# Performance work log

Measured on AMD Instinct MI355X. Metric: run time of the kernel, lower is better.

Reference implementation:

```python
import jax, jax.numpy as jnp
import numpy as np
import math

D_MODEL = 1024
N_HEAD = 16
HEAD_DIM = D_MODEL // N_HEAD
SEQ_LEN = 512
INIT_SIZE = 1568  # from RelativeSinusoidalPositionalEmbedding default


def _rel_pos_embedding(seq_len, embedding_dim):
    # Replicates RelativeSinusoidalPositionalEmbedding with init_size=1568
    num_embeddings = INIT_SIZE + 1  # 1569
    half_dim = embedding_dim // 2
    scale = math.log(10000.0) / (half_dim - 1)
    freqs = np.exp(np.arange(half_dim, dtype=np.float32) * -scale)
    pos = np.arange(-(num_embeddings // 2), num_embeddings // 2, dtype=np.float32)  # [-785, 784)
    emb = pos[:, None] * freqs[None, :]
    weights = np.concatenate([np.sin(emb), np.cos(emb)], axis=1).astype(np.float32)  # (1569, d)
    weights[0, :] = 0.0  # padding_idx
    origin_shift = num_embeddings // 2 + 1  # 785
    positions = np.arange(-seq_len, seq_len) + origin_shift
    embed = weights[positions]  # (2*seq_len, d)
    return jnp.asarray(embed.T)  # (d, 2*seq_len), matching .T in __init__


def setup_inputs() -> dict:
    key = jax.random.key(0)
    k1, k2, k3, k4, k5 = jax.random.split(key, 5)
    x = jax.random.normal(k1, (8, SEQ_LEN, D_MODEL), dtype=jnp.float32)
    prev = jax.random.normal(k2, (8, N_HEAD, SEQ_LEN, SEQ_LEN), dtype=jnp.float32)
    # Linear(d_model, 3*d_model, bias=False): store as (d_model, 3*d_model) for x @ W
    Wqkv = jax.random.normal(k3, (D_MODEL, 3 * D_MODEL), dtype=jnp.float32) / math.sqrt(D_MODEL)
    r_r_bias = jax.random.normal(k4, (1, N_HEAD, 1, HEAD_DIM), dtype=jnp.float32) * 0.02
    r_w_bias = jax.random.normal(k5, (1, N_HEAD, 1, HEAD_DIM), dtype=jnp.float32) * 0.02
    rel_pos = _rel_pos_embedding(SEQ_LEN, HEAD_DIM)  # (head_dim, 2*seq_len)
    return {"x": x, "prev": prev, "Wqkv": Wqkv, "r_r_bias": r_r_bias,
            "r_w_bias": r_w_bias, "rel_pos": rel_pos, "skip_op": 1}


def _shift(BD, seq_len):
    # BD: (b, h, L, 2L) -> (b, h, L, L) via Transformer-XL pad/reshape trick
    b, h, L, two_L = BD.shape
    BD = jnp.pad(BD, ((0, 0), (0, 0), (0, 0), (0, 1)))        # (b,h,L,2L+1)
    BD = BD.reshape(b, h, -1, L)                               # (b,h,2L+1,L)
    BD = BD[:, :, :-1].reshape(b, h, L, -1)                    # (b,h,L,2L)
    return BD[:, :, :, seq_len:]                               # (b,h,L,L)


def reference(x, prev, Wqkv, r_r_bias, r_w_bias, rel_pos, skip_op):
    b, L, d = x.shape
    qkv = x @ Wqkv                                             # (b,L,3d)
    q, k, v = jnp.split(qkv, 3, axis=-1)
    q = q.reshape(b, L, N_HEAD, HEAD_DIM).transpose(0, 2, 1, 3)  # (b,h,L,hd)
    k = k.reshape(b, L, N_HEAD, HEAD_DIM).transpose(0, 2, 1, 3)
    v = v.reshape(b, L, N_HEAD, HEAD_DIM).transpose(0, 2, 1, 3)

    AC = jnp.einsum('bhqd,bhkd->bhqk', q + r_r_bias, k)
    BD = jnp.einsum('bhqd,dp->bhqp', q + r_w_bias, rel_pos)    # (b,h,L,2L)
    BD = _shift(BD, SEQ_LEN)
    E = jnp.einsum('bhkd,dp->bhkp', k, rel_pos)
    E = _shift(E, SEQ_LEN).transpose(0, 1, 3, 2)
    attn_score = (AC + BD + E) / math.sqrt(HEAD_DIM)
    if skip_op:
        attn_score = attn_score + prev
    prev_out = attn_score
    attn = jax.nn.softmax(attn_score, axis=-1)
    out = jnp.einsum('bhqk,bhkd->bhqd', attn, v)
    out = out.transpose(0, 2, 1, 3).reshape(b, L, d)
    return out, prev_out
```

## Files before the change

### kernel.cpp

```cpp
#include <hip/hip_runtime.h>
#include <hip/hip_bf16.h>
#include <math.h>

namespace {
constexpr int Bn = 8;
constexpr int Hn = 16;
constexpr int Ln = 512;
constexpr int HD = 64;
constexpr int DM = 1024;
constexpr int TL = 1024;
constexpr size_t QS  = (size_t)Bn * Hn * Ln * HD;
constexpr size_t FSz = (size_t)Hn * Ln * TL;
constexpr size_t WN  = (size_t)DM * 3 * DM;
}

typedef __bf16 bf16x8 __attribute__((ext_vector_type(8)));
typedef float f32x4 __attribute__((ext_vector_type(4)));

typedef __attribute__((address_space(1))) void as1_void_t;
typedef __attribute__((address_space(3))) void as3_void_t;

__device__ __forceinline__ void gload_lds16(const void* g, void* l) {
  __builtin_amdgcn_global_load_lds((as1_void_t*)g, (as3_void_t*)l, 16, 0, 0);
}

__device__ __forceinline__ unsigned short f2bf(float f) {
  unsigned int u = __float_as_uint(f);
  u += 0x7fffu + ((u >> 16) & 1u);
  return (unsigned short)(u >> 16);
}
__device__ __forceinline__ float bf2f(unsigned short h) {
  return __uint_as_float(((unsigned int)h) << 16);
}

__global__ __launch_bounds__(256) void conv_x(const float* __restrict__ x,
                                              unsigned short* __restrict__ xh,
                                              unsigned short* __restrict__ xl) {
  size_t i = ((size_t)blockIdx.x * 256 + threadIdx.x) * 4;
  float4 v = *(const float4*)(x + i);
  unsigned short h0 = f2bf(v.x), h1 = f2bf(v.y), h2 = f2bf(v.z), h3 = f2bf(v.w);
  ushort4 hv = make_ushort4(h0, h1, h2, h3);
  ushort4 lv = make_ushort4(f2bf(v.x - bf2f(h0)), f2bf(v.y - bf2f(h1)),
                            f2bf(v.z - bf2f(h2)), f2bf(v.w - bf2f(h3)));
  *(ushort4*)(xh + i) = hv;
  *(ushort4*)(xl + i) = lv;
}

__global__ __launch_bounds__(256) void conv_w(const float* __restrict__ W,
                                              unsigned short* __restrict__ wh,
                                              unsigned short* __restrict__ wl) {
  __shared__ unsigned short Th[64][72];
  __shared__ unsigned short Tl[64][72];
  const int t = threadIdx.x;
  const int n0 = blockIdx.x * 64;
  const int k0 = blockIdx.y * 64;
#pragma unroll
  for (int i = 0; i < 4; ++i) {
    int row = i * 16 + (t >> 4);
    int col = (t & 15) * 4;
    float4 v = *(const float4*)(W + (size_t)(k0 + row) * 3072 + n0 + col);
    unsigned short h;
    h = f2bf(v.x); Th[row][col + 0] = h; Tl[row][col + 0] = f2bf(v.x - bf2f(h));
    h = f2bf(v.y); Th[row][col + 1] = h; Tl[row][col + 1] = f2bf(v.y - bf2f(h));
    h = f2bf(v.z); Th[row][col + 2] = h; Tl[row][col + 2] = f2bf(v.z - bf2f(h));
    h = f2bf(v.w); Th[row][col + 3] = h; Tl[row][col + 3] = f2bf(v.w - bf2f(h));
  }
  __syncthreads();
  const int rn = t & 63, qq = t >> 6;
  unsigned int hw[8], lw[8];
#pragma unroll
  for (int j = 0; j < 8; ++j) {
    unsigned short a = Th[qq * 16 + 2 * j][rn], b = Th[qq * 16 + 2 * j + 1][rn];
    hw[j] = (unsigned int)a | ((unsigned int)b << 16);
    unsigned short c = Tl[qq * 16 + 2 * j][rn], d = Tl[qq * 16 + 2 * j + 1][rn];
    lw[j] = (unsigned int)c | ((unsigned int)d << 16);
  }
  size_t o = (size_t)(n0 + rn) * 1024 + k0 + qq * 16;
  *(uint4*)(wh + o)     = make_uint4(hw[0], hw[1], hw[2], hw[3]);
  *(uint4*)(wh + o + 8) = make_uint4(hw[4], hw[5], hw[6], hw[7]);
  *(uint4*)(wl + o)     = make_uint4(lw[0], lw[1], lw[2], lw[3]);
  *(uint4*)(wl + o + 8) = make_uint4(lw[4], lw[5], lw[6], lw[7]);
}

__global__ __launch_bounds__(256, 2) void qkv_mfma(const unsigned short* __restrict__ xh,
                                                   const unsigned short* __restrict__ xl,
                                                   const unsigned short* __restrict__ wh,
                                                   const unsigned short* __restrict__ wl,
                                                   float* __restrict__ qarr,
                                                   float* __restrict__ karr,
                                                   float* __restrict__ varr) {
  __shared__ alignas(16) unsigned short Ah[128 * 32];
  __shared__ alignas(16) unsigned short Al[128 * 32];
  __shared__ alignas(16) unsigned short Bh[128 * 32];
  __shared__ alignas(16) unsigned short Bl[128 * 32];
  const int t = threadIdx.x;
  const int lane = t & 63;
  const int w = t >> 6;
  const int m0 = blockIdx.y * 128;
  const int n0 = blockIdx.x * 128;
  const int wr = w >> 1, wc = w & 1;
  const int l16 = lane & 15, s = lane >> 4;

  const unsigned short* gsrc = (w == 0) ? xh : (w == 1) ? xl : (w == 2) ? wh : wl;
  unsigned short* lbase = (w == 0) ? Ah : (w == 1) ? Al : (w == 2) ? Bh : Bl;
  const int rbase = (w < 2) ? m0 : n0;
  const int srow = lane >> 2, sc = lane & 3;

  int aoff[4], boff[4];
#pragma unroll
  for (int f = 0; f < 4; ++f) {
    int Rm = wr * 64 + f * 16 + l16;
    aoff[f] = Rm * 64 + ((s ^ ((Rm >> 1) & 3)) << 4);
    int Rn = wc * 64 + f * 16 + l16;
    boff[f] = Rn * 64 + ((s ^ ((Rn >> 1) & 3)) << 4);
  }

  f32x4 acc[4][4];
#pragma unroll
  for (int i = 0; i < 4; ++i)
#pragma unroll
    for (int j = 0; j < 4; ++j) acc[i][j] = (f32x4){0.f, 0.f, 0.f, 0.f};

  const char* Ahc = (const char*)Ah;
  const char* Alc = (const char*)Al;
  const char* Bhc = (const char*)Bh;
  const char* Blc = (const char*)Bl;

  for (int k0 = 0; k0 < 1024; k0 += 32) {
#pragma unroll
    for (int u = 0; u < 8; ++u) {
      int row = u * 16 + srow;
      int chunk = sc ^ ((row >> 1) & 3);
      gload_lds16(gsrc + (size_t)(rbase + row) * 1024 + k0 + chunk * 8,
                  lbase + u * 512);
    }
    __syncthreads();

    bf16x8 a_h[4], a_l[4], b_h[4], b_l[4];
#pragma unroll
    for (int f = 0; f < 4; ++f) {
      a_h[f] = *(const bf16x8*)(Ahc + aoff[f]);
      b_h[f] = *(const bf16x8*)(Bhc + boff[f]);
    }
#pragma unroll
    for (int i = 0; i < 4; ++i)
#pragma unroll
      for (int j = 0; j < 4; ++j)
        acc[i][j] = __builtin_amdgcn_mfma_f32_16x16x32_bf16(a_h[i], b_h[j], acc[i][j], 0, 0, 0);
#pragma unroll
    for (int f = 0; f < 4; ++f) b_l[f] = *(const bf16x8*)(Blc + boff[f]);
#pragma unroll
    for (int i = 0; i < 4; ++i)
#pragma unroll
      for (int j = 0; j < 4; ++j)
        acc[i][j] = __builtin_amdgcn_mfma_f32_16x16x32_bf16(a_h[i], b_l[j], acc[i][j], 0, 0, 0);
#pragma unroll
    for (int f = 0; f < 4; ++f) a_l[f] = *(const bf16x8*)(Alc + aoff[f]);
#pragma unroll
    for (int i = 0; i < 4; ++i)
#pragma unroll
      for (int j = 0; j < 4; ++j)
        acc[i][j] = __builtin_amdgcn_mfma_f32_16x16x32_bf16(a_l[i], b_h[j], acc[i][j], 0, 0, 0);
    __syncthreads();
  }

  const int part = n0 >> 10;
  float* dst = (part == 0) ? qarr : (part == 1 ? karr : varr);
  const int nb = n0 & 1023;
#pragma unroll
  for (int i = 0; i < 4; ++i) {
#pragma unroll
    for (int j = 0; j < 4; ++j) {
      const int n = nb + wc * 64 + j * 16 + l16;
      const int h = n >> 6, d = n & 63;
#pragma unroll
      for (int r = 0; r < 4; ++r) {
        int m = m0 + wr * 64 + i * 16 + (lane >> 4) * 4 + r;
        int bb = m >> 9, l = m & 511;
        dst[(((size_t)(bb * Hn + h) * Ln + l) << 6) + d] = acc[i][j][r];
      }
    }
  }
}

__global__ __launch_bounds__(256) void fg_gemm(const float* __restrict__ qarr,
                                               const float* __restrict__ karr,
                                               const float* __restrict__ rwb,
                                               const float* __restrict__ R,
                                               float* __restrict__ F,
                                               float* __restrict__ G,
                                               int b) {
  __shared__ float As[64][68];
  __shared__ float Rs[64][68];
  const int t = threadIdx.x;
  const int h = blockIdx.z >> 1;
  const int which = blockIdx.z & 1;
  const int m0 = blockIdx.y * 64;
  const int n0 = blockIdx.x * 64;
  const float* A = (which == 0 ? qarr : karr) + (size_t)(b * Hn + h) * Ln * HD;

#pragma unroll
  for (int i = 0; i < 4; ++i) {
    int idx = t + i * 256;
    int r = idx >> 4;
    int c4 = (idx & 15) * 4;
    float4 av = *(const float4*)(A + (size_t)(m0 + r) * HD + c4);
    if (which == 0) {
      float4 bv = *(const float4*)(rwb + h * HD + c4);
      av.x += bv.x; av.y += bv.y; av.z += bv.z; av.w += bv.w;
    }
    As[c4 + 0][r] = av.x; As[c4 + 1][r] = av.y;
    As[c4 + 2][r] = av.z; As[c4 + 3][r] = av.w;
    *(float4*)(&Rs[r][c4]) = *(const float4*)(R + (size_t)r * TL + n0 + c4);
  }
  __syncthreads();
  const int tr = t >> 4, tc = t & 15;
  float acc[4][4];
#pragma unroll
  for (int i = 0; i < 4; ++i)
#pragma unroll
    for (int j = 0; j < 4; ++j) acc[i][j] = 0.f;
#pragma unroll 16
  for (int kk = 0; kk < 64; ++kk) {
    float a[4], bb[4];
    *(float4*)(a)  = *(const float4*)(&As[kk][tr * 4]);
    *(float4*)(bb) = *(const float4*)(&Rs[kk][tc * 4]);
#pragma unroll
    for (int i = 0; i < 4; ++i)
#pragma unroll
      for (int j = 0; j < 4; ++j) acc[i][j] = fmaf(a[i], bb[j], acc[i][j]);
  }
  float* O = (which == 0 ? F : G) + ((size_t)h * Ln + m0) * TL + n0;
#pragma unroll
  for (int i = 0; i < 4; ++i) {
    float4 v = make_float4(acc[i][0], acc[i][1], acc[i][2], acc[i][3]);
    *(float4*)(O + (size_t)(tr * 4 + i) * TL + tc * 4) = v;
  }
}

__global__ __launch_bounds__(256) void attn_fused(const float* __restrict__ qarr,
                                                  const float* __restrict__ karr,
                                                  const float* __restrict__ varr,
                                                  const float* __restrict__ rrb,
                                                  const float* __restrict__ F,
                                                  const float* __restrict__ G,
                                                  const float* __restrict__ prev,
                                                  const int* __restrict__ skip,
                                                  float* __restrict__ out,
                                                  float* __restrict__ pout,
                                                  int b) {
  __shared__ float qrT[64][18];
  __shared__ float ktT[64][68];
  __shared__ float vt[64][68];
  __shared__ float St[16][68];
  __shared__ float red[16][16];
  __shared__ float mrun[16], lrun[16], mnew_s[16], alpha_s[16];

  const int t = threadIdx.x;
  const int h = blockIdx.y;
  const int q0 = blockIdx.x * 16;
  const float pf = (skip[0] != 0) ? 1.f : 0.f;
  const size_t bh = (size_t)(b * Hn + h);

  {
    int r = t >> 4, c4 = (t & 15) * 4;
    float4 av = *(const float4*)(qarr + (bh * Ln + q0 + r) * HD + c4);
    float4 bv = *(const float4*)(rrb + h * HD + c4);
    qrT[c4 + 0][r] = av.x + bv.x; qrT[c4 + 1][r] = av.y + bv.y;
    qrT[c4 + 2][r] = av.z + bv.z; qrT[c4 + 3][r] = av.w + bv.w;
  }
  if (t < 16) { mrun[t] = -INFINITY; lrun[t] = 0.f; }

  const int tq = t >> 4, tj = t & 15;
  const int d = t & 63, qg = t >> 6;
  float O[4] = {0.f, 0.f, 0.f, 0.f};

  for (int jt = 0; jt < 8; ++jt) {
    const int j0 = jt * 64;
    __syncthreads();
#pragma unroll
    for (int i = 0; i < 4; ++i) {
      int idx = t + i * 256;
      int r = idx >> 4, c4 = (idx & 15) * 4;
      float4 kv = *(const float4*)(karr + (bh * Ln + j0 + r) * HD + c4);
      ktT[c4 + 0][r] = kv.x; ktT[c4 + 1][r] = kv.y;
      ktT[c4 + 2][r] = kv.z; ktT[c4 + 3][r] = kv.w;
      *(float4*)(&vt[r][c4]) = *(const float4*)(varr + (bh * Ln + j0 + r) * HD + c4);
    }
    __syncthreads();

    float s[4] = {0.f, 0.f, 0.f, 0.f};
#pragma unroll 8
    for (int dd = 0; dd < 64; ++dd) {
      float a = qrT[dd][tq];
      float4 bv = *(const float4*)(&ktT[dd][tj * 4]);
      s[0] = fmaf(a, bv.x, s[0]);
      s[1] = fmaf(a, bv.y, s[1]);
      s[2] = fmaf(a, bv.z, s[2]);
      s[3] = fmaf(a, bv.w, s[3]);
    }
    {
      const int q = q0 + tq;
      const size_t pbase = ((bh * Ln + q) << 9) + j0 + tj * 4;
      float4 pv4 = *(const float4*)(prev + pbase);
      const float pin[4] = {pv4.x, pv4.y, pv4.z, pv4.w};
      float4 o4;
      float* o4p = &o4.x;
#pragma unroll
      for (int ji = 0; ji < 4; ++ji) {
        const int j = j0 + tj * 4 + ji;
        float fv = F[((size_t)h * Ln + q) * TL + (Ln + j - q)];
        float gv = G[((size_t)h * Ln + j) * TL + (Ln + q - j)];
        float sc = (s[ji] + fv + gv) * 0.125f + pf * pin[ji];
        o4p[ji] = sc;
        s[ji] = sc;
        St[tq][tj * 4 + ji] = sc;
      }
      *(float4*)(pout + pbase) = o4;
    }
    __syncthreads();
    {
      const int r = t >> 4, seg = t & 15;
      float mx = St[r][seg * 4];
#pragma unroll
      for (int u = 1; u < 4; ++u) mx = fmaxf(mx, St[r][seg * 4 + u]);
      red[r][seg] = mx;
    }
    __syncthreads();
    if (t < 16) {
      float mx = red[t][0];
#pragma unroll
      for (int u = 1; u < 16; ++u) mx = fmaxf(mx, red[t][u]);
      float mn = fmaxf(mrun[t], mx);
      alpha_s[t] = __expf(mrun[t] - mn);
      mnew_s[t] = mn;
      mrun[t] = mn;
    }
    __syncthreads();
    {
      const float mn = mnew_s[tq];
#pragma unroll
      for (int ji = 0; ji < 4; ++ji) St[tq][tj * 4 + ji] = __expf(s[ji] - mn);
    }
    __syncthreads();
    {
      const int r = t >> 4, seg = t & 15;
      float sm = 0.f;
#pragma unroll
      for (int u = 0; u < 4; ++u) sm += St[r][seg * 4 + u];
      red[r][seg] = sm;
    }
    __syncthreads();
    if (t < 16) {
      float sm = 0.f;
#pragma unroll
      for (int u = 0; u < 16; ++u) sm += red[t][u];
      lrun[t] = lrun[t] * alpha_s[t] + sm;
    }
#pragma unroll
    for (int i = 0; i < 4; ++i) O[i] *= alpha_s[qg * 4 + i];
#pragma unroll 8
    for (int j = 0; j < 64; ++j) {
      float vv = vt[j][d];
#pragma unroll
      for (int i = 0; i < 4; ++i) O[i] = fmaf(St[qg * 4 + i][j], vv, O[i]);
    }
  }
  __syncthreads();
#pragma unroll
  for (int i = 0; i < 4; ++i) {
    int lq = qg * 4 + i;
    float val = O[i] / lrun[lq];
    out[((size_t)b * Ln + q0 + lq) * DM + h * HD + d] = val;
  }
}

extern "C" void kernel_launch(void* const* d_in, const int* in_sizes, int n_in,
                              void* d_out, int out_size, void* d_ws, size_t ws_size,
                              hipStream_t stream) {
  const float* x    = (const float*)d_in[0];
  const float* prev = (const float*)d_in[1];
  const float* W    = (const float*)d_in[2];
  const float* rrb  = (const float*)d_in[3];
  const float* rwb  = (const float*)d_in[4];
  const float* R    = (const float*)d_in[5];
  const int*   skip = (const int*)d_in[6];

  float* out  = (float*)d_out;
  float* pout = out + (size_t)Bn * Ln * DM;

  float* ws = (float*)d_ws;
  float* qarr = ws;
  float* karr = ws + QS;
  float* varr = ws + 2 * QS;
  float* Farr = ws + 3 * QS;
  float* Garr = Farr + FSz;

  unsigned short* xh = (unsigned short*)Farr;
  unsigned short* xl = xh + QS;
  unsigned short* wh = xl + QS;
  unsigned short* wl = wh + WN;

  conv_x<<<dim3(4096), 256, 0, stream>>>(x, xh, xl);
  conv_w<<<dim3(48, 16), 256, 0, stream>>>(W, wh, wl);
  qkv_mfma<<<dim3(24, 32), 256, 0, stream>>>(xh, xl, wh, wl, qarr, karr, varr);
  for (int b = 0; b < Bn; ++b) {
    fg_gemm<<<dim3(TL / 64, Ln / 64, Hn * 2), 256, 0, stream>>>(qarr, karr, rwb, R, Farr, Garr, b);
    attn_fused<<<dim3(Ln / 16, Hn), 256, 0, stream>>>(qarr, karr, varr, rrb, Farr, Garr,
                                                      prev, skip, out, pout, b);
  }
}
```

Baseline: 1.047 ms.

## Store shifted relative-position terms in attention-aligned layout and skip unused tiles

The F/G GEMM now writes its outputs already shifted (and transposed for the key term) into dense (q,j) matrices of size L×L, and blocks whose 64×64 tile falls entirely outside the used diagonal band return early. The attention kernel then reads F and G with coalesced float4 loads instead of scattered diagonal gathers, including a strided column gather for G. The cost moves to scattered, uncoalesced scalar stores in the GEMM epilogue, especially the transposed G writes.

Measured after the change: 1.056 ms. Within noise of the previous version (+0.9%).

```diff
diff --git a/kernel.cpp b/kernel.cpp
--- a/kernel.cpp
+++ b/kernel.cpp
@@ -10,7 +10,7 @@
 constexpr int DM = 1024;
 constexpr int TL = 1024;
 constexpr size_t QS  = (size_t)Bn * Hn * Ln * HD;
-constexpr size_t FSz = (size_t)Hn * Ln * TL;
+constexpr size_t FSz = (size_t)Hn * Ln * Ln;
 constexpr size_t WN  = (size_t)DM * 3 * DM;
 }
 
@@ -187,16 +187,18 @@
                                                const float* __restrict__ karr,
                                                const float* __restrict__ rwb,
                                                const float* __restrict__ R,
-                                               float* __restrict__ F,
-                                               float* __restrict__ G,
+                                               float* __restrict__ Fs,
+                                               float* __restrict__ Gs,
                                                int b) {
+  const int m0 = blockIdx.y * 64;
+  const int n0 = blockIdx.x * 64;
+  if (m0 + n0 + 126 < 512 || m0 + n0 >= 1024) return;
+
   __shared__ float As[64][68];
   __shared__ float Rs[64][68];
   const int t = threadIdx.x;
   const int h = blockIdx.z >> 1;
   const int which = blockIdx.z & 1;
-  const int m0 = blockIdx.y * 64;
-  const int n0 = blockIdx.x * 64;
   const float* A = (which == 0 ? qarr : karr) + (size_t)(b * Hn + h) * Ln * HD;
 
 #pragma unroll
@@ -230,11 +232,30 @@
 #pragma unroll
       for (int j = 0; j < 4; ++j) acc[i][j] = fmaf(a[i], bb[j], acc[i][j]);
   }
-  float* O = (which == 0 ? F : G) + ((size_t)h * Ln + m0) * TL + n0;
-#pragma unroll
-  for (int i = 0; i < 4; ++i) {
-    float4 v = make_float4(acc[i][0], acc[i][1], acc[i][2], acc[i][3]);
-    *(float4*)(O + (size_t)(tr * 4 + i) * TL + tc * 4) = v;
+  if (which == 0) {
+    float* O = Fs + (size_t)h * Ln * Ln;
+#pragma unroll
+    for (int i = 0; i < 4; ++i) {
+      const int q = m0 + tr * 4 + i;
+#pragma unroll
+      for (int jj = 0; jj < 4; ++jj) {
+        const int p = n0 + tc * 4 + jj;
+        const int j = p + q - 512;
+        if ((unsigned)j < 512u) O[((size_t)q << 9) + j] = acc[i][jj];
+      }
+    }
+  } else {
+    float* O = Gs + (size_t)h * Ln * Ln;
+#pragma unroll
+    for (int i = 0; i < 4; ++i) {
+      const int jrow = m0 + tr * 4 + i;
+#pragma unroll
+      for (int jj = 0; jj < 4; ++jj) {
+        const int p = n0 + tc * 4 + jj;
+        const int q = p + jrow - 512;
+        if ((unsigned)q < 512u) O[((size_t)q << 9) + jrow] = acc[i][jj];
+      }
+    }
   }
 }
 
@@ -242,8 +263,8 @@
                                                   const float* __restrict__ karr,
                                                   const float* __restrict__ varr,
                                                   const float* __restrict__ rrb,
-                                                  const float* __restrict__ F,
-                                                  const float* __restrict__ G,
+                                                  const float* __restrict__ Fs,
+                                                  const float* __restrict__ Gs,
                                                   const float* __restrict__ prev,
                                                   const int* __restrict__ skip,
                                                   float* __restrict__ out,
@@ -302,16 +323,18 @@
     {
       const int q = q0 + tq;
       const size_t pbase = ((bh * Ln + q) << 9) + j0 + tj * 4;
+      const size_t fbase = (((size_t)h * Ln + q) << 9) + j0 + tj * 4;
       float4 pv4 = *(const float4*)(prev + pbase);
+      float4 fv4 = *(const float4*)(Fs + fbase);
+      float4 gv4 = *(const float4*)(Gs + fbase);
       const float pin[4] = {pv4.x, pv4.y, pv4.z, pv4.w};
+      const float fin[4] = {fv4.x, fv4.y, fv4.z, fv4.w};
+      const float gin[4] = {gv4.x, gv4.y, gv4.z, gv4.w};
       float4 o4;
       float* o4p = &o4.x;
 #pragma unroll
       for (int ji = 0; ji < 4; ++ji) {
-        const int j = j0 + tj * 4 + ji;
-        float fv = F[((size_t)h * Ln + q) * TL + (Ln + j - q)];
-        float gv = G[((size_t)h * Ln + j) * TL + (Ln + q - j)];
-        float sc = (s[ji] + fv + gv) * 0.125f + pf * pin[ji];
+        float sc = (s[ji] + fin[ji] + gin[ji]) * 0.125f + pf * pin[ji];
         o4p[ji] = sc;
         s[ji] = sc;
         St[tq][tj * 4 + ji] = sc;
```
